# Kernel optimization log

Hardware: AMD Instinct MI355X
Metric: run time of the kernel (lower is better)

Reference implementation:

```python
import math
import jax, jax.numpy as jnp
import numpy as np

E = 1024   # embed_dim
H = 16     # num_heads
DH = E // H
EPS = 1e-8

def round_ste(x):
    # straight-through round (matches brevitas STE behavior)
    return x + jax.lax.stop_gradient(jnp.round(x) - x)

def _scale(x, qmax):
    # dynamic per-tensor abs-max scale (stand-in for brevitas calibrated scale)
    return jnp.maximum(jnp.max(jnp.abs(x)) / qmax, EPS)

def fq(x, s, qmin, qmax):
    # fake-quantize: quantize to int grid, dequantize back to float
    return jnp.clip(round_ste(x / s), qmin, qmax) * s

def quant_linear(x, W, b):
    # Int8ActPerTensorFloat input, Int8WeightPerTensorFloat (narrow range) weight, Int32Bias
    s_x = _scale(x, 128.0)
    s_w = _scale(W, 127.0)
    xq = fq(x, s_x, -128, 127)
    wq = fq(W, s_w, -127, 127)
    y = xq @ wq.T
    if b is not None:
        s_b = s_x * s_w
        y = y + round_ste(b / s_b) * s_b
    return y

def setup_inputs() -> dict:
    k = jax.random.key(0)
    ks = jax.random.split(k, 7)
    S, B = 1024, 4
    return {
        "query": jax.random.normal(ks[0], (S, B, E), jnp.float32),
        "key": jax.random.normal(ks[1], (S, B, E), jnp.float32),
        "value": jax.random.normal(ks[2], (S, B, E), jnp.float32),
        "in_proj_weight": jax.random.normal(ks[3], (3 * E, E), jnp.float32) * 0.02,
        "in_proj_bias": jax.random.normal(ks[4], (3 * E,), jnp.float32) * 0.02,
        "out_proj_weight": jax.random.normal(ks[5], (E, E), jnp.float32) * 0.02,
        "out_proj_bias": jax.random.normal(ks[6], (E,), jnp.float32) * 0.02,
    }

def reference(query, key, value, in_proj_weight, in_proj_bias, out_proj_weight, out_proj_bias):
    S, B, _ = query.shape
    Wq, Wk, Wv = jnp.split(in_proj_weight, 3, axis=0)
    bq, bk, bv = jnp.split(in_proj_bias, 3)
    # quantized QKV projections (packed in_proj split per-input)
    q = quant_linear(query, Wq, bq)   # (S,B,E)
    k = quant_linear(key, Wk, bk)
    v = quant_linear(value, Wv, bv)

    def to_heads(x):  # (S,B,E) -> (B*H, S, DH)
        return x.reshape(S, B * H, DH).transpose(1, 0, 2)

    q = to_heads(q)
    k = to_heads(k)
    v = to_heads(v)

    # q_scaled quant (int8)
    q = q / math.sqrt(DH)
    q = fq(q, _scale(q, 128.0), -128, 127)
    # k_transposed quant (int8)
    kt = k.transpose(0, 2, 1)  # (B*H, DH, S)
    kt = fq(kt, _scale(kt, 128.0), -128, 127)

    attn = q @ kt                      # (B*H, S, S); softmax_input_quant=None -> identity
    attn = jax.nn.softmax(attn, axis=-1)
    # attn_output_weights quant (uint8)
    s_a = jnp.maximum(jnp.max(attn) / 255.0, EPS)
    attn = jnp.clip(round_ste(attn / s_a), 0, 255) * s_a
    # v quant (int8)
    v = fq(v, _scale(v, 128.0), -128, 127)

    out = attn @ v                     # (B*H, S, DH)
    out = out.transpose(1, 0, 2).reshape(S, B, E)
    out = quant_linear(out, out_proj_weight, out_proj_bias)
    return out
```

## Files before the change

### kernel.cpp

```cpp
#include <hip/hip_runtime.h>
#include <stdint.h>

typedef unsigned short u16;
typedef signed char i8;
typedef unsigned char u8;
typedef __attribute__((ext_vector_type(8))) short bf16x8;
typedef __attribute__((ext_vector_type(4))) float f32x4;
typedef __attribute__((ext_vector_type(4))) int i32x4;

#define S_LEN 1024
#define BATCH 4
#define EMB   1024
#define NH    16
#define DHEAD 64
#define BHEAD 64
#define NTOK  4096
#define KDIM  1024
#define NDIM  1024
#define EPSF  1e-8f
#define LOG2E 1.4426950408889634f

#define MFMA16(a,b,c)  __builtin_amdgcn_mfma_f32_16x16x32_bf16((a),(b),(c),0,0,0)
#define MFMAI8(a,b,c)  __builtin_amdgcn_mfma_i32_16x16x64_i8((a),(b),(c),0,0,0)

#define GLOAD16(g, l) __builtin_amdgcn_global_load_lds( \
    (const __attribute__((address_space(1))) void*)(g), \
    (__attribute__((address_space(3))) void*)(l), 16, 0, 0)

#define EXP2F(x) __builtin_amdgcn_exp2f(x)

__device__ __forceinline__ u16 f2bf(float f){
  return (u16)(__float_as_uint(f) >> 16);
}

__device__ __forceinline__ unsigned pack4(float a, float b, float c, float d){
  int qa = (int)a, qb = (int)b, qc = (int)c, qd = (int)d;
  return (unsigned)(qa & 255) | ((unsigned)(qb & 255) << 8) |
         ((unsigned)(qc & 255) << 16) | ((unsigned)(qd & 255) << 24);
}

__device__ __forceinline__ float wave_max(float v){
#pragma unroll
  for (int off = 32; off > 0; off >>= 1) v = fmaxf(v, __shfl_xor(v, off));
  return v;
}


__global__ void k_zero(float* sc){
  if (threadIdx.x < 16) sc[threadIdx.x] = 0.0f;
}

struct AQDesc { const float* x; u8* y; int n4; int slot; float qdiv; float lo; };
struct AQTable { AQDesc d[7]; };

__global__ __launch_bounds__(256) void k_absmax7(AQTable t, int* __restrict__ sci){
  const int bid = blockIdx.x;
  int seg, b0, nb;
  if (bid < 1536){ seg = bid >> 9; b0 = seg << 9; nb = 512; }
  else { seg = 3 + ((bid - 1536) >> 7); b0 = 1536 + ((seg - 3) << 7); nb = 128; }
  const AQDesc D = t.d[seg];
  float m = 0.0f;
  const float4* x4 = (const float4*)D.x;
  for (int i = (bid - b0)*256 + threadIdx.x; i < D.n4; i += nb*256){
    float4 v = x4[i];
    m = fmaxf(m, fmaxf(fmaxf(fabsf(v.x), fabsf(v.y)), fmaxf(fabsf(v.z), fabsf(v.w))));
  }
  m = wave_max(m);
  __shared__ float red[4];
  int lane = threadIdx.x & 63, w = threadIdx.x >> 6;
  if (lane == 0) red[w] = m;
  __syncthreads();
  if (threadIdx.x == 0){
    float mm = fmaxf(fmaxf(red[0], red[1]), fmaxf(red[2], red[3]));
    atomicMax(sci + D.slot, __float_as_int(mm));
  }
}

__global__ __launch_bounds__(256) void k_quant7(AQTable t, const float* __restrict__ sc){
  const int bid = blockIdx.x;
  int seg, b0, nb;
  if (bid < 1536){ seg = bid >> 9; b0 = seg << 9; nb = 512; }
  else { seg = 3 + ((bid - 1536) >> 7); b0 = 1536 + ((seg - 3) << 7); nb = 128; }
  const AQDesc D = t.d[seg];
  const float s = fmaxf(sc[D.slot] / D.qdiv, EPSF);
  const float lo = D.lo;
  const float4* x4 = (const float4*)D.x;
  unsigned* y4 = (unsigned*)D.y;
  for (int i = (bid - b0)*256 + threadIdx.x; i < D.n4; i += nb*256){
    float4 v = x4[i];
    float t0 = fminf(fmaxf(rintf(v.x / s), lo), 127.f);
    float t1 = fminf(fmaxf(rintf(v.y / s), lo), 127.f);
    float t2 = fminf(fmaxf(rintf(v.z / s), lo), 127.f);
    float t3 = fminf(fmaxf(rintf(v.w / s), lo), 127.f);
    y4[i] = pack4(t0, t1, t2, t3);
  }
}

__global__ __launch_bounds__(256) void k_quant(const float* __restrict__ x,
    u8* __restrict__ y, int n4, const float* __restrict__ sc, int slot){
  const float s = fmaxf(sc[slot] / 128.0f, EPSF);
  const float4* x4 = (const float4*)x;
  unsigned* y4 = (unsigned*)y;
  for (int i = blockIdx.x*256 + threadIdx.x; i < n4; i += gridDim.x*256){
    float4 v = x4[i];
    float t0 = fminf(fmaxf(rintf(v.x / s), -128.f), 127.f);
    float t1 = fminf(fmaxf(rintf(v.y / s), -128.f), 127.f);
    float t2 = fminf(fmaxf(rintf(v.z / s), -128.f), 127.f);
    float t3 = fminf(fmaxf(rintf(v.w / s), -128.f), 127.f);
    y4[i] = pack4(t0, t1, t2, t3);
  }
}

__device__ __forceinline__ void gemm_body(const i8* __restrict__ A,
    const i8* __restrict__ W, const float* __restrict__ bias,
    float* __restrict__ out, float s_b, int rowBase, int colBase,
    int* __restrict__ amax_out, i8 (*As)[128], i8 (*Bs)[128], float* red){
  const int tid = threadIdx.x;
  const int wid = tid >> 6, lane = tid & 63;
  const int wm = wid >> 2, wn = wid & 3;
  const int rr = lane & 15, g = lane >> 4;
  const int srow = wid*8 + (lane >> 3);
  const int sco  = ((lane & 7) ^ (lane >> 3)) << 4;
  const i8* Arow0 = &A[(size_t)(rowBase + srow)*KDIM + sco];
  const i8* Arow1 = &A[(size_t)(rowBase + 64 + srow)*KDIM + sco];
  const i8* Wrow0 = &W[(size_t)(colBase + srow)*KDIM + sco];
  const i8* Wrow1 = &W[(size_t)(colBase + 64 + srow)*KDIM + sco];
  i32x4 c[4][2] = {};
  int aoff[4][2], boff[2][2];
#pragma unroll
  for (int i = 0; i < 4; i++){
    int row = wm*64 + i*16 + rr;
#pragma unroll
    for (int h = 0; h < 2; h++)
      aoff[i][h] = row*128 + (((h*4 + g) ^ (row & 7)) << 4);
  }
#pragma unroll
  for (int j = 0; j < 2; j++){
    int row = wn*32 + j*16 + rr;
#pragma unroll
    for (int h = 0; h < 2; h++)
      boff[j][h] = row*128 + (((h*4 + g) ^ (row & 7)) << 4);
  }
  for (int k0 = 0; k0 < KDIM; k0 += 128){
    __syncthreads();
    GLOAD16(Arow0 + k0, &As[wid*8][0]);
    GLOAD16(Arow1 + k0, &As[64 + wid*8][0]);
    GLOAD16(Wrow0 + k0, &Bs[wid*8][0]);
    GLOAD16(Wrow1 + k0, &Bs[64 + wid*8][0]);
    __syncthreads();
#pragma unroll
    for (int h = 0; h < 2; h++){
      i32x4 af[4], bfr[2];
#pragma unroll
      for (int i = 0; i < 4; i++) af[i]  = *(const i32x4*)((const i8*)As + aoff[i][h]);
#pragma unroll
      for (int j = 0; j < 2; j++) bfr[j] = *(const i32x4*)((const i8*)Bs + boff[j][h]);
#pragma unroll
      for (int i = 0; i < 4; i++)
#pragma unroll
        for (int j = 0; j < 2; j++)
          c[i][j] = MFMAI8(af[i], bfr[j], c[i][j]);
    }
  }
  float lmax = 0.0f;
  const int r0 = (lane >> 4) * 4, ccol = lane & 15;
#pragma unroll
  for (int j = 0; j < 2; j++){
    int col = colBase + wn*32 + j*16 + ccol;
    float rb = rintf(bias[col] / s_b);
#pragma unroll
    for (int i = 0; i < 4; i++){
      int rowb = rowBase + wm*64 + i*16 + r0;
#pragma unroll
      for (int rI = 0; rI < 4; rI++){
        float y = s_b * ((float)c[i][j][rI] + rb);
        out[(size_t)(rowb + rI)*NDIM + col] = y;
        lmax = fmaxf(lmax, fabsf(y));
      }
    }
  }
  lmax = wave_max(lmax);
  if (lane == 0) red[wid] = lmax;
  __syncthreads();
  if (tid == 0){
    float mm = red[0];
#pragma unroll
    for (int i2 = 1; i2 < 8; i2++) mm = fmaxf(mm, red[i2]);
    atomicMax(amax_out, __float_as_int(mm));
  }
}

__global__ __launch_bounds__(512) void k_gemm3(const i8* __restrict__ Xall,
    const i8* __restrict__ Wall, const float* __restrict__ ball,
    float* __restrict__ Yall, const float* __restrict__ sc, int* __restrict__ sci){
  __shared__ i8 As[128][128];
  __shared__ i8 Bs[128][128];
  __shared__ float red[8];
  const int orig = blockIdx.x;
  const int xcd = orig & 7, sl = orig >> 3;
  const int seg = sl >> 5;
  const int t2 = xcd*32 + (sl & 31);
  const int by = t2 >> 3, bx = t2 & 7;
  const float s_x = fmaxf(sc[seg] / 128.0f, EPSF);
  const float s_w = fmaxf(sc[3 + seg] / 127.0f, EPSF);
  gemm_body(Xall + (size_t)seg*NTOK*KDIM, Wall + (size_t)seg*KDIM*NDIM,
            ball + seg*1024, Yall + (size_t)seg*NTOK*NDIM, s_x*s_w,
            by*128, bx*128, sci + 7 + seg, As, Bs, red);
}

__global__ __launch_bounds__(512) void k_gemm1(const i8* __restrict__ A,
    const i8* __restrict__ W, const float* __restrict__ bias,
    float* __restrict__ out, const float* __restrict__ sc,
    int sx_slot, int sw_slot, int* __restrict__ amax_out){
  __shared__ i8 As[128][128];
  __shared__ i8 Bs[128][128];
  __shared__ float red[8];
  const int orig = blockIdx.x;
  const int t2 = (orig & 7)*32 + (orig >> 3);
  const int by = t2 >> 3, bx = t2 & 7;
  const float s_x = fmaxf(sc[sx_slot] / 128.0f, EPSF);
  const float s_w = fmaxf(sc[sw_slot] / 127.0f, EPSF);
  gemm_body(A, W, bias, out, s_x*s_w, by*128, bx*128, amax_out, As, Bs, red);
}

__global__ __launch_bounds__(256) void k_quant_heads(const float* __restrict__ qf,
    const float* __restrict__ kf, const float* __restrict__ vf,
    i8* __restrict__ qh, i8* __restrict__ kh, u16* __restrict__ vt,
    const float* __restrict__ sc){
  const float s_q = fmaxf((sc[7]*0.125f)/128.0f, EPSF);
  const float s_k = fmaxf(sc[8]/128.0f, EPSF);
  const float s_v = fmaxf(sc[9]/128.0f, EPSF);
  __shared__ u16 tile[64][80];
  const int bx = blockIdx.x;
  const int st = bx & 15, hh = (bx >> 4) & 15, b = bx >> 8;
  const int t = threadIdx.x;
  const int sl = t >> 2, dc = (t & 3) * 16;
  const size_t row = (size_t)(st*64 + sl)*BATCH + b;
  const size_t ibase = row*EMB + hh*DHEAD + dc;
  const int bh = b*NH + hh;
  float vq[16], vk[16], vv[16];
#pragma unroll
  for (int i = 0; i < 4; i++){
    *(float4*)&vq[i*4] = *(const float4*)&qf[ibase + i*4];
    *(float4*)&vk[i*4] = *(const float4*)&kf[ibase + i*4];
    *(float4*)&vv[i*4] = *(const float4*)&vf[ibase + i*4];
  }
  alignas(16) i8 oq[16], ok[16];
#pragma unroll
  for (int i = 0; i < 16; i++){
    float tq = fminf(fmaxf(rintf((vq[i]*0.125f)/s_q), -128.f), 127.f);
    float tk = fminf(fmaxf(rintf(vk[i]/s_k), -128.f), 127.f);
    float tv = fminf(fmaxf(rintf(vv[i]/s_v), -128.f), 127.f);
    oq[i] = (i8)(int)tq; ok[i] = (i8)(int)tk;
    tile[dc + i][sl] = f2bf(tv);
  }
  const size_t qoff = ((size_t)bh*S_LEN + st*64 + sl)*DHEAD + dc;
  *(int4*)&qh[qoff] = *(const int4*)&oq[0];
  *(int4*)&kh[qoff] = *(const int4*)&ok[0];
  __syncthreads();
  const int d = t >> 2, sc4 = (t & 3) * 16;
  alignas(16) u16 ov[16];
#pragma unroll
  for (int i = 0; i < 16; i++) ov[i] = tile[d][sc4 + i];
  const size_t voff = ((size_t)bh*DHEAD + d)*S_LEN + st*64 + sc4;
  *(bf16x8*)&vt[voff]     = *(const bf16x8*)&ov[0];
  *(bf16x8*)&vt[voff + 8] = *(const bf16x8*)&ov[8];
}

__global__ __launch_bounds__(256) void k_attn1(const i8* __restrict__ qh,
    const i8* __restrict__ kh, float* __restrict__ mrow, float* __restrict__ lrow,
    const float* __restrict__ sc, int* __restrict__ sci){
  __shared__ i8 Ks[64][64];
  __shared__ float red2[4];
  const int orig = blockIdx.x;
  const int tile = (orig & 7) * 128 + (orig >> 3);
  const int bhead = tile >> 4, q0 = (tile & 15) * 64;
  const int tid = threadIdx.x, w = tid >> 6, lane = tid & 63;
  const int rr = lane & 15, g = lane >> 4;
  const float s_q = fmaxf((sc[7]*0.125f)/128.0f, EPSF);
  const float s_k = fmaxf(sc[8]/128.0f, EPSF);
  const float s_qk = s_q * s_k;
  const i8* qbase = qh + ((size_t)bhead*S_LEN + q0 + w*16)*DHEAD;
  const i8* kbase = kh + (size_t)bhead*S_LEN*DHEAD;
  i32x4 a = *(const i32x4*)&qbase[rr*DHEAD + g*16];
  const int srow = w*16 + (lane >> 2);
  const int sco  = ((lane & 3) ^ ((srow >> 1) & 3)) << 4;
  float m[4] = {-1e30f, -1e30f, -1e30f, -1e30f};
  float l[4] = {0.f, 0.f, 0.f, 0.f};
  for (int cch = 0; cch < 16; cch++){
    const int n0 = cch * 64;
    __syncthreads();
    GLOAD16(&kbase[(size_t)(n0 + srow)*DHEAD + sco], &Ks[w*16][0]);
    __syncthreads();
    float sv[4][4];
#pragma unroll
    for (int nt = 0; nt < 4; nt++){
      int row = nt*16 + rr;
      i32x4 b = *(const i32x4*)((const i8*)Ks + row*64 + (((g ^ ((row >> 1) & 3))) << 4));
      i32x4 acc = {};
      acc = MFMAI8(a, b, acc);
#pragma unroll
      for (int r = 0; r < 4; r++) sv[nt][r] = (float)acc[r]*s_qk;
    }
#pragma unroll
    for (int r = 0; r < 4; r++){
      float cm = fmaxf(fmaxf(sv[0][r], sv[1][r]), fmaxf(sv[2][r], sv[3][r]));
      float mn = fmaxf(m[r], cm);
      l[r] *= EXP2F((m[r] - mn)*LOG2E);
      m[r] = mn;
#pragma unroll
      for (int nt = 0; nt < 4; nt++)
        l[r] += EXP2F((sv[nt][r] - m[r])*LOG2E);
    }
  }
#pragma unroll
  for (int off = 1; off < 16; off <<= 1){
#pragma unroll
    for (int r = 0; r < 4; r++){
      float mo = __shfl_xor(m[r], off), lo = __shfl_xor(l[r], off);
      float mn = fmaxf(m[r], mo);
      l[r] = l[r]*EXP2F((m[r] - mn)*LOG2E) + lo*EXP2F((mo - mn)*LOG2E);
      m[r] = mn;
    }
  }
  if (rr == 0){
    int rowb = q0 + w*16 + g*4;
#pragma unroll
    for (int r = 0; r < 4; r++){
      mrow[(size_t)bhead*S_LEN + rowb + r] = m[r];
      lrow[(size_t)bhead*S_LEN + rowb + r] = l[r];
    }
  }
  float im = 0.0f;
#pragma unroll
  for (int r = 0; r < 4; r++) im = fmaxf(im, 1.0f / l[r]);
  im = wave_max(im);
  if (lane == 0) red2[w] = im;
  __syncthreads();
  if (tid == 0){
    float mm = fmaxf(fmaxf(red2[0], red2[1]), fmaxf(red2[2], red2[3]));
    atomicMax(sci + 13, __float_as_int(mm));
  }
}

__global__ void k_sa_final(float* sc, const int* sci){
  if (threadIdx.x == 0)
    sc[11] = fmaxf(__int_as_float(sci[13]) / 255.0f, EPSF);
}

__global__ __launch_bounds__(256) void k_attn2(const i8* __restrict__ qh,
    const i8* __restrict__ kh, const u16* __restrict__ vt,
    const float* __restrict__ mrow, const float* __restrict__ lrow,
    float* __restrict__ aout, const float* __restrict__ sc, int* __restrict__ amax_out){
  __shared__ i8 Ks[64][64];
  __shared__ u16 Vs[64][64];
  __shared__ u16 P[4][16][72];
  __shared__ float red[4];
  const int orig = blockIdx.x;
  const int tile = (orig & 7) * 128 + (orig >> 3);
  const int bhead = tile >> 4, q0 = (tile & 15) * 64;
  const int tid = threadIdx.x, w = tid >> 6, lane = tid & 63;
  const int rr = lane & 15, g = lane >> 4, kk = g * 8;
  const int lr3 = lane >> 3, lc = lane & 7;
  const float s_q = fmaxf((sc[7]*0.125f)/128.0f, EPSF);
  const float s_k = fmaxf(sc[8]/128.0f, EPSF);
  const float s_qk = s_q * s_k;
  const float s_v = fmaxf(sc[9]/128.0f, EPSF);
  const float s_a = sc[11];
  const float fac = s_a * s_v;
  const i8* qbase = qh + ((size_t)bhead*S_LEN + q0 + w*16)*DHEAD;
  const i8* kbase = kh + (size_t)bhead*S_LEN*DHEAD;
  const u16* vbase = vt + (size_t)bhead*DHEAD*S_LEN;
  i32x4 a = *(const i32x4*)&qbase[rr*DHEAD + g*16];
  float mr[4], inv[4];
  {
    int rowb = q0 + w*16 + g*4;
#pragma unroll
    for (int r = 0; r < 4; r++){
      mr[r]  = mrow[(size_t)bhead*S_LEN + rowb + r];
      inv[r] = 1.0f / (lrow[(size_t)bhead*S_LEN + rowb + r] * s_a);
    }
  }
  const int srow = w*16 + (lane >> 2);
  const int sco  = ((lane & 3) ^ ((srow >> 1) & 3)) << 4;
  f32x4 cpv[4] = {};
  for (int cch = 0; cch < 16; cch++){
    const int n0 = cch * 64;
    __syncthreads();
    GLOAD16(&kbase[(size_t)(n0 + srow)*DHEAD + sco], &Ks[w*16][0]);
#pragma unroll
    for (int i = 0; i < 2; i++){
      int d = w*16 + i*8 + lr3;
      GLOAD16(&vbase[(size_t)d*S_LEN + n0 + ((lc ^ (d & 7)) << 3)], &Vs[w*16 + i*8][0]);
    }
    __syncthreads();
#pragma unroll
    for (int nt = 0; nt < 4; nt++){
      int row = nt*16 + rr;
      i32x4 b = *(const i32x4*)((const i8*)Ks + row*64 + (((g ^ ((row >> 1) & 3))) << 4));
      i32x4 acc = {};
      acc = MFMAI8(a, b, acc);
#pragma unroll
      for (int r = 0; r < 4; r++){
        float e  = EXP2F(((float)acc[r]*s_qk - mr[r])*LOG2E);
        float pq = fminf(rintf(e * inv[r]), 255.0f);
        P[w][g*4 + r][nt*16 + rr] = f2bf(pq);
      }
    }
    bf16x8 pa0 = *(const bf16x8*)&P[w][rr][kk];
    bf16x8 pa1 = *(const bf16x8*)&P[w][rr][32 + kk];
#pragma unroll
    for (int f = 0; f < 4; f++){
      int row = f*16 + rr;
      bf16x8 v0 = *(const bf16x8*)((const u16*)Vs + row*64 + (((g    ) ^ (row & 7)) << 3));
      bf16x8 v1 = *(const bf16x8*)((const u16*)Vs + row*64 + (((4 + g) ^ (row & 7)) << 3));
      cpv[f] = MFMA16(pa0, v0, cpv[f]);
      cpv[f] = MFMA16(pa1, v1, cpv[f]);
    }
  }
  const int b = bhead >> 4, hh = bhead & 15;
  float lmax = 0.0f;
#pragma unroll
  for (int f = 0; f < 4; f++){
    int d = f*16 + rr;
#pragma unroll
    for (int r = 0; r < 4; r++){
      int srow2 = q0 + w*16 + g*4 + r;
      float y = fac * cpv[f][r];
      aout[(size_t)(srow2*BATCH + b)*EMB + hh*DHEAD + d] = y;
      lmax = fmaxf(lmax, fabsf(y));
    }
  }
  lmax = wave_max(lmax);
  __syncthreads();
  if (lane == 0) red[w] = lmax;
  __syncthreads();
  if (tid == 0){
    float mm = fmaxf(fmaxf(red[0], red[1]), fmaxf(red[2], red[3]));
    atomicMax(amax_out, __float_as_int(mm));
  }
}

extern "C" void kernel_launch(void* const* d_in, const int* in_sizes, int n_in,
                              void* d_out, int out_size, void* d_ws, size_t ws_size,
                              hipStream_t stream){
  const float* query = (const float*)d_in[0];
  const float* key   = (const float*)d_in[1];
  const float* value = (const float*)d_in[2];
  const float* inW   = (const float*)d_in[3];
  const float* inB   = (const float*)d_in[4];
  const float* outW  = (const float*)d_in[5];
  const float* outB  = (const float*)d_in[6];
  float* out = (float*)d_out;

  char* ws = (char*)d_ws;
  float* sc  = (float*)ws;
  int*   sci = (int*)ws;
  u8* WQQ = (u8*)(ws + 256);
  u8* WKQ = WQQ + 1024*1024;
  u8* WVQ = WKQ + 1024*1024;
  u8* WOQ = WVQ + 1024*1024;
  u8* XQ  = WOQ + 1024*1024;
  u8* XK  = XQ + (size_t)NTOK*1024;
  u8* XV  = XK + (size_t)NTOK*1024;
  float* QF = (float*)(XV + (size_t)NTOK*1024);
  float* KF = QF + (size_t)NTOK*1024;
  float* VF = KF + (size_t)NTOK*1024;
  u16* VT = (u16*)(VF + (size_t)NTOK*1024);
  float* MROW = (float*)(VT + (size_t)BHEAD*DHEAD*S_LEN);
  float* LROW = MROW + BHEAD*S_LEN;
  i8* QH  = (i8*)XQ;   i8* KH = (i8*)XK;
  float* AOUT = QF;
  u8* AOQ = XV;

  AQTable tab;
  tab.d[0] = { query,             XQ,  NTOK*1024/4, 0, 128.f, -128.f };
  tab.d[1] = { key,               XK,  NTOK*1024/4, 1, 128.f, -128.f };
  tab.d[2] = { value,             XV,  NTOK*1024/4, 2, 128.f, -128.f };
  tab.d[3] = { inW,               WQQ, 1024*1024/4, 3, 127.f, -127.f };
  tab.d[4] = { inW + 1024*1024,   WKQ, 1024*1024/4, 4, 127.f, -127.f };
  tab.d[5] = { inW + 2*1024*1024, WVQ, 1024*1024/4, 5, 127.f, -127.f };
  tab.d[6] = { outW,              WOQ, 1024*1024/4, 6, 127.f, -127.f };

  k_zero<<<1, 64, 0, stream>>>(sc);
  k_absmax7<<<2048, 256, 0, stream>>>(tab, sci);
  k_quant7<<<2048, 256, 0, stream>>>(tab, sc);
  k_gemm3<<<768, 512, 0, stream>>>((const i8*)XQ, (const i8*)WQQ, inB, QF, sc, sci);
  k_quant_heads<<<1024, 256, 0, stream>>>(QF, KF, VF, QH, KH, VT, sc);
  k_attn1<<<1024, 256, 0, stream>>>(QH, KH, MROW, LROW, sc, sci);
  k_sa_final<<<1, 64, 0, stream>>>(sc, sci);
  k_attn2<<<1024, 256, 0, stream>>>(QH, KH, VT, MROW, LROW, AOUT, sc, sci + 10);
  k_quant<<<1024, 256, 0, stream>>>(AOUT, AOQ, NTOK*1024/4, sc, 10);
  k_gemm1<<<256, 512, 0, stream>>>((const i8*)AOQ, (const i8*)WOQ, outB, out, sc, 10, 6, sci + 12);
}
```

Baseline: 187.7 us.

## Switch P·V to int8 MFMA with offset-corrected probabilities and fold log2e

Stores transposed V as int8 instead of bf16 and shifts quantized attention probabilities (0..255) by -128 so the P·V product runs on the int8 16x16x64 MFMA. The shift is undone exactly by adding 128 times a per-(head,d) column sum of V, computed with atomics in the head-quantization kernel. The change also folds LOG2E into the score scale constant, uses an fma for the exponent argument, and removes the single-thread s_a finalize launch by computing s_a inline. It halves V traffic and shared-memory footprint and cuts MFMA count, at the cost of extra atomics and a larger zeroing kernel.

Result: slower. 191.6 us (+2.0%).

```diff
diff --git a/kernel.cpp b/kernel.cpp
--- a/kernel.cpp
+++ b/kernel.cpp
@@ -20,7 +20,6 @@
 #define EPSF  1e-8f
 #define LOG2E 1.4426950408889634f
 
-#define MFMA16(a,b,c)  __builtin_amdgcn_mfma_f32_16x16x32_bf16((a),(b),(c),0,0,0)
 #define MFMAI8(a,b,c)  __builtin_amdgcn_mfma_i32_16x16x64_i8((a),(b),(c),0,0,0)
 
 #define GLOAD16(g, l) __builtin_amdgcn_global_load_lds( \
@@ -28,10 +27,6 @@
     (__attribute__((address_space(3))) void*)(l), 16, 0, 0)
 
 #define EXP2F(x) __builtin_amdgcn_exp2f(x)
-
-__device__ __forceinline__ u16 f2bf(float f){
-  return (u16)(__float_as_uint(f) >> 16);
-}
 
 __device__ __forceinline__ unsigned pack4(float a, float b, float c, float d){
   int qa = (int)a, qb = (int)b, qc = (int)c, qd = (int)d;
@@ -46,8 +41,12 @@
 }
 
 
-__global__ void k_zero(float* sc){
-  if (threadIdx.x < 16) sc[threadIdx.x] = 0.0f;
+__global__ __launch_bounds__(256) void k_zero(float* sc, int* vtot){
+  if (blockIdx.x == 0){
+    if (threadIdx.x < 16) sc[threadIdx.x] = 0.0f;
+  } else {
+    vtot[(blockIdx.x - 1)*256 + threadIdx.x] = 0;
+  }
 }
 
 struct AQDesc { const float* x; u8* y; int n4; int slot; float qdiv; float lo; };
@@ -225,12 +224,12 @@
 
 __global__ __launch_bounds__(256) void k_quant_heads(const float* __restrict__ qf,
     const float* __restrict__ kf, const float* __restrict__ vf,
-    i8* __restrict__ qh, i8* __restrict__ kh, u16* __restrict__ vt,
-    const float* __restrict__ sc){
+    i8* __restrict__ qh, i8* __restrict__ kh, i8* __restrict__ vt,
+    int* __restrict__ vtot, const float* __restrict__ sc){
   const float s_q = fmaxf((sc[7]*0.125f)/128.0f, EPSF);
   const float s_k = fmaxf(sc[8]/128.0f, EPSF);
   const float s_v = fmaxf(sc[9]/128.0f, EPSF);
-  __shared__ u16 tile[64][80];
+  __shared__ i8 tile[64][68];
   const int bx = blockIdx.x;
   const int st = bx & 15, hh = (bx >> 4) & 15, b = bx >> 8;
   const int t = threadIdx.x;
@@ -252,19 +251,27 @@
     float tk = fminf(fmaxf(rintf(vk[i]/s_k), -128.f), 127.f);
     float tv = fminf(fmaxf(rintf(vv[i]/s_v), -128.f), 127.f);
     oq[i] = (i8)(int)tq; ok[i] = (i8)(int)tk;
-    tile[dc + i][sl] = f2bf(tv);
+    tile[dc + i][sl] = (i8)(int)tv;
   }
   const size_t qoff = ((size_t)bh*S_LEN + st*64 + sl)*DHEAD + dc;
   *(int4*)&qh[qoff] = *(const int4*)&oq[0];
   *(int4*)&kh[qoff] = *(const int4*)&ok[0];
   __syncthreads();
   const int d = t >> 2, sc4 = (t & 3) * 16;
-  alignas(16) u16 ov[16];
-#pragma unroll
-  for (int i = 0; i < 16; i++) ov[i] = tile[d][sc4 + i];
+  int ovi[4];
+  int sum = 0;
+#pragma unroll
+  for (int w4 = 0; w4 < 4; w4++){
+    unsigned x = *(const unsigned*)&tile[d][sc4 + w4*4];
+    ovi[w4] = (int)x;
+#pragma unroll
+    for (int bb = 0; bb < 4; bb++) sum += (int)(i8)(x >> (8*bb));
+  }
   const size_t voff = ((size_t)bh*DHEAD + d)*S_LEN + st*64 + sc4;
-  *(bf16x8*)&vt[voff]     = *(const bf16x8*)&ov[0];
-  *(bf16x8*)&vt[voff + 8] = *(const bf16x8*)&ov[8];
+  *(int4*)&vt[voff] = *(const int4*)&ovi[0];
+  sum += __shfl_xor(sum, 1);
+  sum += __shfl_xor(sum, 2);
+  if ((t & 3) == 0) atomicAdd(&vtot[bh*DHEAD + d], sum);
 }
 
 __global__ __launch_bounds__(256) void k_attn1(const i8* __restrict__ qh,
@@ -279,7 +286,7 @@
   const int rr = lane & 15, g = lane >> 4;
   const float s_q = fmaxf((sc[7]*0.125f)/128.0f, EPSF);
   const float s_k = fmaxf(sc[8]/128.0f, EPSF);
-  const float s_qk = s_q * s_k;
+  const float C1 = s_q * s_k * LOG2E;
   const i8* qbase = qh + ((size_t)bhead*S_LEN + q0 + w*16)*DHEAD;
   const i8* kbase = kh + (size_t)bhead*S_LEN*DHEAD;
   i32x4 a = *(const i32x4*)&qbase[rr*DHEAD + g*16];
@@ -300,17 +307,17 @@
       i32x4 acc = {};
       acc = MFMAI8(a, b, acc);
 #pragma unroll
-      for (int r = 0; r < 4; r++) sv[nt][r] = (float)acc[r]*s_qk;
+      for (int r = 0; r < 4; r++) sv[nt][r] = (float)acc[r]*C1;
     }
 #pragma unroll
     for (int r = 0; r < 4; r++){
       float cm = fmaxf(fmaxf(sv[0][r], sv[1][r]), fmaxf(sv[2][r], sv[3][r]));
       float mn = fmaxf(m[r], cm);
-      l[r] *= EXP2F((m[r] - mn)*LOG2E);
+      l[r] *= EXP2F(m[r] - mn);
       m[r] = mn;
 #pragma unroll
       for (int nt = 0; nt < 4; nt++)
-        l[r] += EXP2F((sv[nt][r] - m[r])*LOG2E);
+        l[r] += EXP2F(sv[nt][r] - m[r]);
     }
   }
 #pragma unroll
@@ -319,7 +326,7 @@
     for (int r = 0; r < 4; r++){
       float mo = __shfl_xor(m[r], off), lo = __shfl_xor(l[r], off);
       float mn = fmaxf(m[r], mo);
-      l[r] = l[r]*EXP2F((m[r] - mn)*LOG2E) + lo*EXP2F((mo - mn)*LOG2E);
+      l[r] = l[r]*EXP2F(m[r] - mn) + lo*EXP2F(mo - mn);
       m[r] = mn;
     }
   }
@@ -343,56 +350,49 @@
   }
 }
 
-__global__ void k_sa_final(float* sc, const int* sci){
-  if (threadIdx.x == 0)
-    sc[11] = fmaxf(__int_as_float(sci[13]) / 255.0f, EPSF);
-}
-
 __global__ __launch_bounds__(256) void k_attn2(const i8* __restrict__ qh,
-    const i8* __restrict__ kh, const u16* __restrict__ vt,
+    const i8* __restrict__ kh, const i8* __restrict__ vt,
     const float* __restrict__ mrow, const float* __restrict__ lrow,
-    float* __restrict__ aout, const float* __restrict__ sc, int* __restrict__ amax_out){
+    const int* __restrict__ vtot, float* __restrict__ aout,
+    const float* __restrict__ sc, const int* __restrict__ sci,
+    int* __restrict__ amax_out){
   __shared__ i8 Ks[64][64];
-  __shared__ u16 Vs[64][64];
-  __shared__ u16 P[4][16][72];
+  __shared__ i8 Vs[64][64];
+  __shared__ i8 P[4][16][68];
   __shared__ float red[4];
   const int orig = blockIdx.x;
   const int tile = (orig & 7) * 128 + (orig >> 3);
   const int bhead = tile >> 4, q0 = (tile & 15) * 64;
   const int tid = threadIdx.x, w = tid >> 6, lane = tid & 63;
-  const int rr = lane & 15, g = lane >> 4, kk = g * 8;
-  const int lr3 = lane >> 3, lc = lane & 7;
+  const int rr = lane & 15, g = lane >> 4;
   const float s_q = fmaxf((sc[7]*0.125f)/128.0f, EPSF);
   const float s_k = fmaxf(sc[8]/128.0f, EPSF);
-  const float s_qk = s_q * s_k;
+  const float C1 = s_q * s_k * LOG2E;
   const float s_v = fmaxf(sc[9]/128.0f, EPSF);
-  const float s_a = sc[11];
+  const float s_a = fmaxf(__int_as_float(sci[13]) / 255.0f, EPSF);
   const float fac = s_a * s_v;
   const i8* qbase = qh + ((size_t)bhead*S_LEN + q0 + w*16)*DHEAD;
   const i8* kbase = kh + (size_t)bhead*S_LEN*DHEAD;
-  const u16* vbase = vt + (size_t)bhead*DHEAD*S_LEN;
+  const i8* vbase = vt + (size_t)bhead*DHEAD*S_LEN;
   i32x4 a = *(const i32x4*)&qbase[rr*DHEAD + g*16];
-  float mr[4], inv[4];
+  float nm[4], inv[4];
   {
     int rowb = q0 + w*16 + g*4;
 #pragma unroll
     for (int r = 0; r < 4; r++){
-      mr[r]  = mrow[(size_t)bhead*S_LEN + rowb + r];
+      nm[r]  = -mrow[(size_t)bhead*S_LEN + rowb + r];
       inv[r] = 1.0f / (lrow[(size_t)bhead*S_LEN + rowb + r] * s_a);
     }
   }
   const int srow = w*16 + (lane >> 2);
   const int sco  = ((lane & 3) ^ ((srow >> 1) & 3)) << 4;
-  f32x4 cpv[4] = {};
+  const int vco  = (lane & 3) << 4;
+  i32x4 cpv[4] = {};
   for (int cch = 0; cch < 16; cch++){
     const int n0 = cch * 64;
     __syncthreads();
     GLOAD16(&kbase[(size_t)(n0 + srow)*DHEAD + sco], &Ks[w*16][0]);
-#pragma unroll
-    for (int i = 0; i < 2; i++){
-      int d = w*16 + i*8 + lr3;
-      GLOAD16(&vbase[(size_t)d*S_LEN + n0 + ((lc ^ (d & 7)) << 3)], &Vs[w*16 + i*8][0]);
-    }
+    GLOAD16(&vbase[(size_t)srow*S_LEN + n0 + vco], &Vs[w*16][0]);
     __syncthreads();
 #pragma unroll
     for (int nt = 0; nt < 4; nt++){
@@ -402,20 +402,24 @@
       acc = MFMAI8(a, b, acc);
 #pragma unroll
       for (int r = 0; r < 4; r++){
-        float e  = EXP2F(((float)acc[r]*s_qk - mr[r])*LOG2E);
-        float pq = fminf(rintf(e * inv[r]), 255.0f);
-        P[w][g*4 + r][nt*16 + rr] = f2bf(pq);
+        float arg = fmaf((float)acc[r], C1, nm[r]);
+        float e   = EXP2F(arg);
+        float pq  = fminf(rintf(e * inv[r]), 255.0f);
+        P[w][g*4 + r][nt*16 + rr] = (i8)((int)pq - 128);
       }
     }
-    bf16x8 pa0 = *(const bf16x8*)&P[w][rr][kk];
-    bf16x8 pa1 = *(const bf16x8*)&P[w][rr][32 + kk];
+    i32x4 pa;
+    {
+      const i8* pptr = &P[w][rr][g*16];
+      pa[0] = *(const int*)(pptr + 0);
+      pa[1] = *(const int*)(pptr + 4);
+      pa[2] = *(const int*)(pptr + 8);
+      pa[3] = *(const int*)(pptr + 12);
+    }
 #pragma unroll
     for (int f = 0; f < 4; f++){
-      int row = f*16 + rr;
-      bf16x8 v0 = *(const bf16x8*)((const u16*)Vs + row*64 + (((g    ) ^ (row & 7)) << 3));
-      bf16x8 v1 = *(const bf16x8*)((const u16*)Vs + row*64 + (((4 + g) ^ (row & 7)) << 3));
-      cpv[f] = MFMA16(pa0, v0, cpv[f]);
-      cpv[f] = MFMA16(pa1, v1, cpv[f]);
+      i32x4 bv = *(const i32x4*)&Vs[f*16 + rr][g*16];
+      cpv[f] = MFMAI8(pa, bv, cpv[f]);
     }
   }
   const int b = bhead >> 4, hh = bhead & 15;
@@ -423,10 +427,11 @@
 #pragma unroll
   for (int f = 0; f < 4; f++){
     int d = f*16 + rr;
+    int vcorr = 128 * vtot[bhead*DHEAD + d];
 #pragma unroll
     for (int r = 0; r < 4; r++){
       int srow2 = q0 + w*16 + g*4 + r;
-      float y = fac * cpv[f][r];
+      float y = fac * (float)(cpv[f][r] + vcorr);
       aout[(size_t)(srow2*BATCH + b)*EMB + hh*DHEAD + d] = y;
       lmax = fmaxf(lmax, fabsf(y));
     }
@@ -456,7 +461,8 @@
   char* ws = (char*)d_ws;
   float* sc  = (float*)ws;
   int*   sci = (int*)ws;
-  u8* WQQ = (u8*)(ws + 256);
+  int*   vtotI = (int*)(ws + 256);
+  u8* WQQ = (u8*)(ws + 256 + 16384);
   u8* WKQ = WQQ + 1024*1024;
   u8* WVQ = WKQ + 1024*1024;
   u8* WOQ = WVQ + 1024*1024;
@@ -466,7 +472,7 @@
   float* QF = (float*)(XV + (size_t)NTOK*1024);
   float* KF = QF + (size_t)NTOK*1024;
   float* VF = KF + (size_t)NTOK*1024;
-  u16* VT = (u16*)(VF + (size_t)NTOK*1024);
+  i8* VT = (i8*)(VF + (size_t)NTOK*1024);
   float* MROW = (float*)(VT + (size_t)BHEAD*DHEAD*S_LEN);
   float* LROW = MROW + BHEAD*S_LEN;
   i8* QH  = (i8*)XQ;   i8* KH = (i8*)XK;
@@ -482,14 +488,13 @@
   tab.d[5] = { inW + 2*1024*1024, WVQ, 1024*1024/4, 5, 127.f, -127.f };
   tab.d[6] = { outW,              WOQ, 1024*1024/4, 6, 127.f, -127.f };
 
-  k_zero<<<1, 64, 0, stream>>>(sc);
+  k_zero<<<17, 256, 0, stream>>>(sc, vtotI);
   k_absmax7<<<2048, 256, 0, stream>>>(tab, sci);
   k_quant7<<<2048, 256, 0, stream>>>(tab, sc);
   k_gemm3<<<768, 512, 0, stream>>>((const i8*)XQ, (const i8*)WQQ, inB, QF, sc, sci);
-  k_quant_heads<<<1024, 256, 0, stream>>>(QF, KF, VF, QH, KH, VT, sc);
+  k_quant_heads<<<1024, 256, 0, stream>>>(QF, KF, VF, QH, KH, VT, vtotI, sc);
   k_attn1<<<1024, 256, 0, stream>>>(QH, KH, MROW, LROW, sc, sci);
-  k_sa_final<<<1, 64, 0, stream>>>(sc, sci);
-  k_attn2<<<1024, 256, 0, stream>>>(QH, KH, VT, MROW, LROW, AOUT, sc, sci + 10);
+  k_attn2<<<1024, 256, 0, stream>>>(QH, KH, VT, MROW, LROW, vtotI, AOUT, sc, sci, sci + 10);
   k_quant<<<1024, 256, 0, stream>>>(AOUT, AOQ, NTOK*1024/4, sc, 10);
   k_gemm1<<<256, 512, 0, stream>>>((const i8*)AOQ, (const i8*)WOQ, outB, out, sc, 10, 6, sci + 12);
 }
```
